# Kernel optimization log

Hardware: AMD Instinct MI355X
Metric: run time of the kernel (lower is better)

## Reference

```python
import jax, jax.numpy as jnp
import numpy as np
import math

EMBED_DIM = 1024
NUM_HEADS = 16
HEAD_DIM = EMBED_DIM // NUM_HEADS
WINDOW_SIZE = 512
BATCH = 2
SEQ_LEN = 2048


def setup_inputs() -> dict:
    key = jax.random.key(0)
    ks = jax.random.split(key, 9)
    s = 1.0 / math.sqrt(EMBED_DIM)
    inp = {
        "x": jax.random.normal(ks[0], (BATCH, SEQ_LEN, EMBED_DIM), dtype=jnp.float32),
        "Wq": jax.random.normal(ks[1], (EMBED_DIM, EMBED_DIM), dtype=jnp.float32) * s,
        "bq": jnp.zeros((EMBED_DIM,), dtype=jnp.float32),
        "Wk": jax.random.normal(ks[2], (EMBED_DIM, EMBED_DIM), dtype=jnp.float32) * s,
        "bk": jnp.zeros((EMBED_DIM,), dtype=jnp.float32),
        "Wv": jax.random.normal(ks[3], (EMBED_DIM, EMBED_DIM), dtype=jnp.float32) * s,
        "bv": jnp.zeros((EMBED_DIM,), dtype=jnp.float32),
        "Wo": jax.random.normal(ks[4], (EMBED_DIM, EMBED_DIM), dtype=jnp.float32) * s,
        "bo": jnp.zeros((EMBED_DIM,), dtype=jnp.float32),
    }
    return inp


def _sliding_window_mask(seq_len: int, window_size: int) -> jnp.ndarray:
    # mask[i, j] = 0 if |i - j| <= window_size // 2 else -inf
    i = jnp.arange(seq_len)[:, None]
    j = jnp.arange(seq_len)[None, :]
    allowed = jnp.abs(i - j) <= (window_size // 2)
    return jnp.where(allowed, 0.0, -jnp.inf).astype(jnp.float32)


def _split_heads(t):
    b, s, d = t.shape
    return t.reshape(b, s, NUM_HEADS, HEAD_DIM).transpose(0, 2, 1, 3)  # [b,h,s,hd]


def reference(x, Wq, bq, Wk, bk, Wv, bv, Wo, bo):
    b, s, d = x.shape
    q = _split_heads(x @ Wq + bq)
    k = _split_heads(x @ Wk + bk)
    v = _split_heads(x @ Wv + bv)
    # dense QK^T + additive sliding-window mask + softmax + PV (as in source)
    scores = jnp.einsum("bhqd,bhkd->bhqk", q, k) / math.sqrt(HEAD_DIM)
    scores = scores + _sliding_window_mask(s, WINDOW_SIZE)
    probs = jax.nn.softmax(scores, axis=-1)
    attn = jnp.einsum("bhqk,bhkd->bhqd", probs, v)
    attn = attn.transpose(0, 2, 1, 3).reshape(b, s, d)  # merge heads
    return attn @ Wo + bo
```

## Files before the change

### kernel.cpp

```cpp
#include <hip/hip_runtime.h>
#include <math.h>
#include <stdint.h>

#define BATCH 2
#define SEQ   2048
#define EMB   1024
#define NHEADS 16
#define HDIM  64
#define WHALF 256

typedef __attribute__((ext_vector_type(8))) short short8;
typedef __attribute__((ext_vector_type(8))) _Float16 half8;
typedef __attribute__((ext_vector_type(4))) _Float16 half4;
typedef __attribute__((ext_vector_type(4))) float f32x4;

__global__ __launch_bounds__(256)
void cast16_kernel(const float* __restrict__ in, unsigned short* __restrict__ o16, int n)
{
    const int i = (blockIdx.x * 256 + threadIdx.x) * 8;
    if (i >= n) return;
    float4 v0 = *(const float4*)&in[i];
    float4 v1 = *(const float4*)&in[i + 4];
    half8 h;
    h[0] = (_Float16)v0.x; h[1] = (_Float16)v0.y;
    h[2] = (_Float16)v0.z; h[3] = (_Float16)v0.w;
    h[4] = (_Float16)v1.x; h[5] = (_Float16)v1.y;
    h[6] = (_Float16)v1.z; h[7] = (_Float16)v1.w;
    *(half8*)&o16[i] = h;
}

__global__ __launch_bounds__(256)
void wsplit16_t_kernel(const float* __restrict__ W0, const float* __restrict__ W1,
                       const float* __restrict__ W2, const float* __restrict__ W3,
                       unsigned short* __restrict__ o16)
{
    __shared__ float t[32][33];
    const float* W = (blockIdx.z == 0) ? W0 : (blockIdx.z == 1) ? W1
                   : (blockIdx.z == 2) ? W2 : W3;
    const float scale = (blockIdx.z == 0) ? 0.125f : 1.0f;
    const int n0 = blockIdx.x * 32;
    const int k0 = blockIdx.y * 32;
    const int tx = threadIdx.x & 31, ty = threadIdx.x >> 5;
#pragma unroll
    for (int i = 0; i < 4; ++i)
        t[ty + i * 8][tx] = W[(size_t)(k0 + ty + i * 8) * EMB + n0 + tx];
    __syncthreads();
#pragma unroll
    for (int i = 0; i < 4; ++i) {
        float v = t[tx][ty + i * 8] * scale;
        size_t o = (size_t)(blockIdx.z * EMB + n0 + ty + i * 8) * EMB + k0 + tx;
        *(_Float16*)&o16[o] = (_Float16)v;
    }
}

__global__ __launch_bounds__(256)
void bias_cat_kernel(const float* __restrict__ bq, const float* __restrict__ bk,
                     const float* __restrict__ bv, float* __restrict__ out)
{
    const int i = blockIdx.x * 256 + threadIdx.x;
    if (i < 1024)      out[i] = bq[i] * 0.125f;
    else if (i < 2048) out[i] = bk[i - 1024];
    else if (i < 3072) out[i] = bv[i - 2048];
}

#define GLDS(gp, lp) __builtin_amdgcn_global_load_lds(                       \
    (const __attribute__((address_space(1))) void*)(gp),                     \
    (__attribute__((address_space(3))) void*)(lp), 16, 0, 0)

#define TRS 136

__global__ __launch_bounds__(256)
void gemm_f16_qkv_kernel(const unsigned short* __restrict__ A,
                         const unsigned short* __restrict__ B,
                         const float* __restrict__ bias,
                         _Float16* __restrict__ QK,
                         _Float16* __restrict__ Vt, int K)
{
    __shared__ __align__(16) unsigned short smem[128 * TRS];
    unsigned short* sA = smem;
    unsigned short* sB = smem + 4096;
    _Float16* tr = (_Float16*)smem;

    const int tid = threadIdx.x;
    const int l = tid & 63;
    const int w = tid >> 6;
    const int wm = w >> 1, wn = w & 1;
    const int row0 = blockIdx.y * 128;
    const int col0 = blockIdx.x * 128;

    f32x4 acc[4][4] = {};

    const int sr = tid >> 2;
    const int sk = (tid & 3) * 8;
    const unsigned short* pA = A + (size_t)(row0 + sr) * K + sk;
    const unsigned short* pB = B + (size_t)(col0 + sr) * K + sk;
    const size_t rstep = (size_t)64 * K;

    const int kq = (l >> 4) * 8;
    const int lr = l & 15;
    const int lq = l >> 4;

    for (int k0 = 0; k0 < K; k0 += 32) {
        GLDS(pA + k0,         &sA[tid * 8]);
        GLDS(pA + rstep + k0, &sA[2048 + tid * 8]);
        GLDS(pB + k0,         &sB[tid * 8]);
        GLDS(pB + rstep + k0, &sB[2048 + tid * 8]);
        __syncthreads();

        half8 af[4], bf[4];
#pragma unroll
        for (int f = 0; f < 4; ++f) {
            af[f] = *(const half8*)&sA[(wm * 64 + f * 16 + lr) * 32 + kq];
            bf[f] = *(const half8*)&sB[(wn * 64 + f * 16 + lr) * 32 + kq];
        }
#pragma unroll
        for (int mf = 0; mf < 4; ++mf)
#pragma unroll
            for (int nf = 0; nf < 4; ++nf)
                acc[mf][nf] = __builtin_amdgcn_mfma_f32_16x16x32_f16(af[mf], bf[nf], acc[mf][nf], 0, 0, 0);
        __syncthreads();
    }

    if (col0 < 2048) {
#pragma unroll
        for (int nf = 0; nf < 4; ++nf) {
            const int c = wn * 64 + nf * 16 + lr;
            const float bv = bias[col0 + c];
#pragma unroll
            for (int mf = 0; mf < 4; ++mf) {
                const int rl = wm * 64 + mf * 16 + lq * 4;
#pragma unroll
                for (int i = 0; i < 4; ++i)
                    tr[(rl + i) * TRS + c] = (_Float16)(acc[mf][nf][i] + bv);
            }
        }
        __syncthreads();
        const int r = tid >> 1, seg = (tid & 1) * 64;
        _Float16* dst = QK + (size_t)(row0 + r) * 2048 + col0 + seg;
#pragma unroll
        for (int t = 0; t < 8; ++t)
            *(half8*)&dst[t * 8] = *(const half8*)&tr[r * TRS + seg + t * 8];
    } else {
#pragma unroll
        for (int nf = 0; nf < 4; ++nf) {
            const int c = wn * 64 + nf * 16 + lr;
            const float bv = bias[col0 + c];
#pragma unroll
            for (int mf = 0; mf < 4; ++mf) {
                const int rl = wm * 64 + mf * 16 + lq * 4;
#pragma unroll
                for (int i = 0; i < 4; ++i)
                    tr[c * TRS + rl + i] = (_Float16)(acc[mf][nf][i] + bv);
            }
        }
        __syncthreads();
        const int c = tid >> 1, seg = (tid & 1) * 64;
        const int vb = row0 >> 11;
        const int s0 = (row0 & 2047) + seg;
        _Float16* dst = Vt + ((size_t)(vb * 1024 + (col0 - 2048) + c)) * 2048 + s0;
#pragma unroll
        for (int t = 0; t < 8; ++t)
            *(half8*)&dst[t * 8] = *(const half8*)&tr[c * TRS + seg + t * 8];
    }
}

__global__ __launch_bounds__(256)
void gemm_f16_m64_kernel(const unsigned short* __restrict__ A,
                         const unsigned short* __restrict__ B,
                         const float* __restrict__ bias,
                         float* __restrict__ C, int ldc, int K)
{
    __shared__ unsigned short sA[64 * 32], sB[128 * 32];

    const int tid = threadIdx.x;
    const int l = tid & 63;
    const int w = tid >> 6;
    const int wm = w >> 1, wn = w & 1;
    const int row0 = blockIdx.y * 64;
    const int col0 = blockIdx.x * 128;

    f32x4 acc[2][4] = {};

    const int sr = tid >> 2;
    const int sk = (tid & 3) * 8;
    const unsigned short* pA = A + (size_t)(row0 + sr) * K + sk;
    const unsigned short* pB = B + (size_t)(col0 + sr) * K + sk;
    const size_t rstep = (size_t)64 * K;

    const int kq = (l >> 4) * 8;
    const int lr = l & 15;
    const int lq = l >> 4;

    for (int k0 = 0; k0 < K; k0 += 32) {
        GLDS(pA + k0,         &sA[tid * 8]);
        GLDS(pB + k0,         &sB[tid * 8]);
        GLDS(pB + rstep + k0, &sB[2048 + tid * 8]);
        __syncthreads();

        half8 af[2], bf[4];
#pragma unroll
        for (int f = 0; f < 2; ++f)
            af[f] = *(const half8*)&sA[(wm * 32 + f * 16 + lr) * 32 + kq];
#pragma unroll
        for (int f = 0; f < 4; ++f)
            bf[f] = *(const half8*)&sB[(wn * 64 + f * 16 + lr) * 32 + kq];
#pragma unroll
        for (int mf = 0; mf < 2; ++mf)
#pragma unroll
            for (int nf = 0; nf < 4; ++nf)
                acc[mf][nf] = __builtin_amdgcn_mfma_f32_16x16x32_f16(af[mf], bf[nf], acc[mf][nf], 0, 0, 0);
        __syncthreads();
    }

#pragma unroll
    for (int nf = 0; nf < 4; ++nf) {
        const int c = wn * 64 + nf * 16 + lr;
        const float bv = bias[col0 + c];
#pragma unroll
        for (int mf = 0; mf < 2; ++mf) {
            const int r = row0 + wm * 32 + mf * 16 + lq * 4;
#pragma unroll
            for (int i = 0; i < 4; ++i)
                C[(size_t)(r + i) * ldc + col0 + c] = acc[mf][nf][i] + bv;
        }
    }
}

#define AP 66

__global__ __launch_bounds__(512)
void attn_f16_kernel(const unsigned short* __restrict__ QKb,
                     const unsigned short* __restrict__ Vt,
                     unsigned short* __restrict__ Oa)
{
    __shared__ unsigned short Qs[128 * AP], Ks[64 * AP], Vs[64 * AP], Ps[128 * AP];

    const int tid = threadIdx.x;
    const int gid = blockIdx.x;
    const int X = gid & 7, rest = gid >> 3;
    const int hg = rest & 3, tile = rest >> 2;
    const int bh = X * 4 + hg;
    const int b = bh >> 4, h = bh & 15;
    const int q0 = tile * 128;

    const int l = tid & 63, w = tid >> 6;
    const int lr = l & 15, g = l >> 4;

    const size_t rowbase = (size_t)b * SEQ;

    {
        const int r = tid >> 2, sg = (tid & 3) * 16;
        const unsigned short* src = QKb + (rowbase + q0 + r) * 2048 + h * HDIM + sg;
        *(short8*)&Qs[r * AP + sg]     = *(const short8*)src;
        *(short8*)&Qs[r * AP + sg + 8] = *(const short8*)(src + 8);
    }
    __syncthreads();

    half8 qa0 = *(const half8*)&Qs[(w * 16 + lr) * AP + g * 8];
    half8 qa1 = *(const half8*)&Qs[(w * 16 + lr) * AP + 32 + g * 8];

    f32x4 o[4] = {};
    float m_ = -1e30f, l_ = 0.0f;
    const int q = q0 + w * 16 + lr;

    const int c_begin = (q0 >= WHALF) ? 0 : (WHALF - q0) >> 6;
    int c_end = (SEQ + 255 - q0) >> 6; if (c_end > 9) c_end = 9;

    for (int c = c_begin; c <= c_end; ++c) {
        const int cs = q0 - WHALF + c * 64;

        {
            const int r = tid >> 3, sg = (tid & 7) * 8;
            const unsigned short* ks = QKb + (rowbase + cs + r) * 2048 + 1024 + h * HDIM + sg;
            *(short8*)&Ks[r * AP + sg] = *(const short8*)ks;
            const unsigned short* vs = Vt + ((size_t)(b * 1024 + h * HDIM + r)) * 2048 + cs + sg;
            *(short8*)&Vs[r * AP + sg] = *(const short8*)vs;
        }
        __syncthreads();

        f32x4 sc[4] = {};
#pragma unroll
        for (int kf = 0; kf < 4; ++kf) {
            half8 a0 = *(const half8*)&Ks[(kf * 16 + lr) * AP + g * 8];
            half8 a1 = *(const half8*)&Ks[(kf * 16 + lr) * AP + 32 + g * 8];
            sc[kf] = __builtin_amdgcn_mfma_f32_16x16x32_f16(a0, qa0, sc[kf], 0, 0, 0);
            sc[kf] = __builtin_amdgcn_mfma_f32_16x16x32_f16(a1, qa1, sc[kf], 0, 0, 0);
        }

        if (c <= 1) {
#pragma unroll
            for (int kf = 0; kf < 4; ++kf)
#pragma unroll
                for (int i = 0; i < 4; ++i) {
                    const int key = cs + kf * 16 + g * 4 + i;
                    if (key < q - WHALF) sc[kf][i] = -1e30f;
                }
        } else if (c >= 8) {
#pragma unroll
            for (int kf = 0; kf < 4; ++kf)
#pragma unroll
                for (int i = 0; i < 4; ++i) {
                    const int key = cs + kf * 16 + g * 4 + i;
                    if (key > q + WHALF) sc[kf][i] = -1e30f;
                }
        }

        float cm = sc[0][0];
#pragma unroll
        for (int kf = 0; kf < 4; ++kf)
#pragma unroll
            for (int i = 0; i < 4; ++i) cm = fmaxf(cm, sc[kf][i]);
        cm = fmaxf(cm, __shfl_xor(cm, 16));
        cm = fmaxf(cm, __shfl_xor(cm, 32));

        const float mn = fmaxf(fmaxf(m_, cm), -1e4f);
        const float alpha = __expf(m_ - mn);
        m_ = mn;

        float rs = 0.0f;
#pragma unroll
        for (int kf = 0; kf < 4; ++kf) {
            half4 pk;
#pragma unroll
            for (int i = 0; i < 4; ++i) {
                const float p = __expf(sc[kf][i] - mn);
                rs += p;
                pk[i] = (_Float16)p;
            }
            *(half4*)&Ps[(w * 16 + lr) * AP + kf * 16 + g * 4] = pk;
        }
        rs += __shfl_xor(rs, 16);
        rs += __shfl_xor(rs, 32);
        l_ = l_ * alpha + rs;

        float al[4];
#pragma unroll
        for (int i = 0; i < 4; ++i)
            al[i] = __shfl(alpha, (l & 48) | (g * 4 + i));
#pragma unroll
        for (int df = 0; df < 4; ++df)
#pragma unroll
            for (int i = 0; i < 4; ++i) o[df][i] *= al[i];

        half8 pa0 = *(const half8*)&Ps[(w * 16 + lr) * AP + g * 8];
        half8 pa1 = *(const half8*)&Ps[(w * 16 + lr) * AP + 32 + g * 8];
#pragma unroll
        for (int df = 0; df < 4; ++df) {
            half8 vb0 = *(const half8*)&Vs[(df * 16 + lr) * AP + g * 8];
            half8 vb1 = *(const half8*)&Vs[(df * 16 + lr) * AP + 32 + g * 8];
            o[df] = __builtin_amdgcn_mfma_f32_16x16x32_f16(pa0, vb0, o[df], 0, 0, 0);
            o[df] = __builtin_amdgcn_mfma_f32_16x16x32_f16(pa1, vb1, o[df], 0, 0, 0);
        }
        __syncthreads();
    }

    float invl[4];
#pragma unroll
    for (int i = 0; i < 4; ++i)
        invl[i] = 1.0f / __shfl(l_, (l & 48) | (g * 4 + i));
#pragma unroll
    for (int df = 0; df < 4; ++df)
#pragma unroll
        for (int i = 0; i < 4; ++i) {
            const float v = o[df][i] * invl[i];
            const size_t off = (rowbase + q0 + w * 16 + g * 4 + i) * 1024
                             + h * HDIM + df * 16 + lr;
            *(_Float16*)&Oa[off] = (_Float16)v;
        }
}

#define BM 64
#define BN 64
#define BK 16

__global__ __launch_bounds__(256)
void gemm_bias_kernel(const float* __restrict__ A, const float* __restrict__ W,
                      const float* __restrict__ bias, float* __restrict__ C,
                      int M, int N, int K)
{
    __shared__ float As[BK][BM + 4];
    __shared__ float Bs[BK][BN + 4];
    const int tid = threadIdx.x;
    const int tx = tid & 15, ty = tid >> 4;
    const int row0 = blockIdx.y * BM;
    const int col0 = blockIdx.x * BN;
    float acc[4][4] = {};
    const int ar = tid >> 2;
    const int ak = (tid & 3) * 4;
    const int br = tid >> 4;
    const int bc = (tid & 15) * 4;
    for (int k0 = 0; k0 < K; k0 += BK) {
        float4 a = *(const float4*)&A[(size_t)(row0 + ar) * K + k0 + ak];
        float4 b = *(const float4*)&W[(size_t)(k0 + br) * N + col0 + bc];
        As[ak + 0][ar] = a.x; As[ak + 1][ar] = a.y;
        As[ak + 2][ar] = a.z; As[ak + 3][ar] = a.w;
        *(float4*)&Bs[br][bc] = b;
        __syncthreads();
#pragma unroll
        for (int kk = 0; kk < BK; ++kk) {
            float4 av = *(const float4*)&As[kk][ty * 4];
            float4 bv = *(const float4*)&Bs[kk][tx * 4];
            float aa[4] = {av.x, av.y, av.z, av.w};
            float bb[4] = {bv.x, bv.y, bv.z, bv.w};
#pragma unroll
            for (int i = 0; i < 4; ++i)
#pragma unroll
                for (int j = 0; j < 4; ++j)
                    acc[i][j] = fmaf(aa[i], bb[j], acc[i][j]);
        }
        __syncthreads();
    }
    const float4 bvec = *(const float4*)&bias[col0 + tx * 4];
    const float bb[4] = {bvec.x, bvec.y, bvec.z, bvec.w};
#pragma unroll
    for (int i = 0; i < 4; ++i) {
        float4 oo;
        oo.x = acc[i][0] + bb[0]; oo.y = acc[i][1] + bb[1];
        oo.z = acc[i][2] + bb[2]; oo.w = acc[i][3] + bb[3];
        *(float4*)&C[(size_t)(row0 + ty * 4 + i) * N + col0 + tx * 4] = oo;
    }
}

#define QT 32
#define KT 64

__global__ __launch_bounds__(256)
void attn_kernel(const float* __restrict__ Qm, int ldq,
                 const float* __restrict__ Km, int ldk,
                 const float* __restrict__ Vm, int ldv,
                 float* __restrict__ Om, int ldo)
{
    __shared__ float Qs[QT][HDIM + 4];
    __shared__ float KVs[KT][HDIM + 4];
    __shared__ float Ps[QT][KT + 1];
    __shared__ float red[8][QT];
    __shared__ float m_s[QT], l_s[QT], alpha_s[QT];
    const int tid = threadIdx.x;
    const int b  = blockIdx.y / NHEADS;
    const int h  = blockIdx.y % NHEADS;
    const int q0 = blockIdx.x * QT;
    const int r  = tid & 31;
    const int cg = tid >> 5;
    const int d0 = cg * 8;
    {
        const int qr = tid >> 3;
        const int qd = (tid & 7) * 8;
        const float* src = Qm + (size_t)(b * SEQ + q0 + qr) * ldq + h * HDIM + qd;
        *(float4*)&Qs[qr][qd]     = *(const float4*)(src);
        *(float4*)&Qs[qr][qd + 4] = *(const float4*)(src + 4);
    }
    if (tid < QT) { m_s[tid] = -1e30f; l_s[tid] = 0.0f; }
    __syncthreads();
    float qreg[HDIM];
#pragma unroll
    for (int d4 = 0; d4 < HDIM; d4 += 4) {
        float4 t = *(const float4*)&Qs[r][d4];
        qreg[d4] = t.x; qreg[d4 + 1] = t.y; qreg[d4 + 2] = t.z; qreg[d4 + 3] = t.w;
    }
    float o[8] = {};
    const int iq = q0 + r;
    int lo = q0 - WHALF; if (lo < 0) lo = 0;
    const int cs0 = lo & ~(KT - 1);
    int hi = q0 + QT + WHALF; if (hi > SEQ) hi = SEQ;
    const int nch = (hi - cs0 + KT - 1) / KT;
    const int kr0 = tid >> 4;
    const int kc  = (tid & 15) * 4;
    for (int ch = 0; ch < nch; ++ch) {
        const int cs = cs0 + ch * KT;
#pragma unroll
        for (int r4 = 0; r4 < 4; ++r4) {
            const int row = kr0 + r4 * 16;
            const int j = cs + row;
            float4 v = make_float4(0.f, 0.f, 0.f, 0.f);
            if (j < SEQ)
                v = *(const float4*)&Km[(size_t)(b * SEQ + j) * ldk + h * HDIM + kc];
            *(float4*)&KVs[row][kc] = v;
        }
        __syncthreads();
        float s[8];
#pragma unroll
        for (int cc = 0; cc < 8; ++cc) {
            const int cidx = d0 + cc;
            float acc = 0.0f;
#pragma unroll
            for (int d4 = 0; d4 < HDIM; d4 += 4) {
                float4 kv = *(const float4*)&KVs[cidx][d4];
                acc = fmaf(qreg[d4],     kv.x, acc);
                acc = fmaf(qreg[d4 + 1], kv.y, acc);
                acc = fmaf(qreg[d4 + 2], kv.z, acc);
                acc = fmaf(qreg[d4 + 3], kv.w, acc);
            }
            const int j = cs + cidx;
            const bool valid = (j < SEQ) && (j >= iq - WHALF) && (j <= iq + WHALF);
            s[cc] = valid ? acc * 0.125f : -1e30f;
        }
        float lm = s[0];
#pragma unroll
        for (int cc = 1; cc < 8; ++cc) lm = fmaxf(lm, s[cc]);
        red[cg][r] = lm;
        __syncthreads();
        if (tid < QT) {
            float m = m_s[tid];
            float mc = red[0][tid];
#pragma unroll
            for (int g2 = 1; g2 < 8; ++g2) mc = fmaxf(mc, red[g2][tid]);
            const float mn = fmaxf(m, mc);
            alpha_s[tid] = __expf(m - mn);
            m_s[tid] = mn;
        }
        __syncthreads();
        const float mn = m_s[r];
        float ls = 0.0f;
#pragma unroll
        for (int cc = 0; cc < 8; ++cc) {
            const float p = __expf(s[cc] - mn);
            Ps[r][d0 + cc] = p;
            ls += p;
        }
        red[cg][r] = ls;
        __syncthreads();
        if (tid < QT) {
            float sum = red[0][tid];
#pragma unroll
            for (int g2 = 1; g2 < 8; ++g2) sum += red[g2][tid];
            l_s[tid] = l_s[tid] * alpha_s[tid] + sum;
        }
#pragma unroll
        for (int r4 = 0; r4 < 4; ++r4) {
            const int row = kr0 + r4 * 16;
            const int j = cs + row;
            float4 v = make_float4(0.f, 0.f, 0.f, 0.f);
            if (j < SEQ)
                v = *(const float4*)&Vm[(size_t)(b * SEQ + j) * ldv + h * HDIM + kc];
            *(float4*)&KVs[row][kc] = v;
        }
        {
            const float al = alpha_s[r];
#pragma unroll
            for (int dd = 0; dd < 8; ++dd) o[dd] *= al;
        }
        __syncthreads();
        for (int j = 0; j < KT; ++j) {
            const float p = Ps[r][j];
            float4 v0 = *(const float4*)&KVs[j][d0];
            float4 v1 = *(const float4*)&KVs[j][d0 + 4];
            o[0] = fmaf(p, v0.x, o[0]); o[1] = fmaf(p, v0.y, o[1]);
            o[2] = fmaf(p, v0.z, o[2]); o[3] = fmaf(p, v0.w, o[3]);
            o[4] = fmaf(p, v1.x, o[4]); o[5] = fmaf(p, v1.y, o[5]);
            o[6] = fmaf(p, v1.z, o[6]); o[7] = fmaf(p, v1.w, o[7]);
        }
        __syncthreads();
    }
    const float inv = 1.0f / l_s[r];
    float4 o0, o1;
    o0.x = o[0] * inv; o0.y = o[1] * inv; o0.z = o[2] * inv; o0.w = o[3] * inv;
    o1.x = o[4] * inv; o1.y = o[5] * inv; o1.z = o[6] * inv; o1.w = o[7] * inv;
    float* dst = Om + (size_t)(b * SEQ + q0 + r) * ldo + h * HDIM + d0;
    *(float4*)dst       = o0;
    *(float4*)(dst + 4) = o1;
}

extern "C" void kernel_launch(void* const* d_in, const int* in_sizes, int n_in,
                              void* d_out, int out_size, void* d_ws, size_t ws_size,
                              hipStream_t stream)
{
    const float* x  = (const float*)d_in[0];
    const float* Wq = (const float*)d_in[1];
    const float* bq = (const float*)d_in[2];
    const float* Wk = (const float*)d_in[3];
    const float* bk = (const float*)d_in[4];
    const float* Wv = (const float*)d_in[5];
    const float* bv = (const float*)d_in[6];
    const float* Wo = (const float*)d_in[7];
    const float* bo = (const float*)d_in[8];
    float* out = (float*)d_out;

    const int M = BATCH * SEQ;
    const size_t MK = (size_t)M * EMB;

    const size_t need = ((size_t)40 << 20) + 16384;
    dim3 blk(256);

    if (ws_size >= need) {
        unsigned short* Wh  = (unsigned short*)d_ws;
        unsigned short* xh  = Wh + (size_t)4096 * EMB;
        unsigned short* QKb = xh + MK;
        unsigned short* Vt  = QKb + (size_t)4096 * 2048;
        unsigned short* Oa  = xh;
        float* bias_cat = (float*)((char*)d_ws + ((size_t)40 << 20));

        hipLaunchKernelGGL(cast16_kernel, dim3((int)(MK / (256 * 8))), blk, 0, stream,
                           x, xh, (int)MK);
        hipLaunchKernelGGL(wsplit16_t_kernel, dim3(32, 32, 4), blk, 0, stream,
                           Wq, Wk, Wv, Wo, Wh);
        hipLaunchKernelGGL(bias_cat_kernel, dim3(12), blk, 0, stream, bq, bk, bv, bias_cat);

        hipLaunchKernelGGL(gemm_f16_qkv_kernel, dim3(24, 32), blk, 0, stream,
                           xh, Wh, bias_cat, (_Float16*)QKb, (_Float16*)Vt, EMB);

        hipLaunchKernelGGL(attn_f16_kernel, dim3(512), dim3(512), 0, stream, QKb, Vt, Oa);

        hipLaunchKernelGGL(gemm_f16_m64_kernel, dim3(8, 64), blk, 0, stream,
                           Oa, Wh + (size_t)3072 * EMB, bo, out, EMB, EMB);
    } else {
        float* Qb = (float*)d_ws;
        float* Kb = Qb + MK;
        float* Vb = out;
        dim3 ggrid(EMB / BN, M / BM);
        hipLaunchKernelGGL(gemm_bias_kernel, ggrid, blk, 0, stream, x, Wq, bq, Qb, M, EMB, EMB);
        hipLaunchKernelGGL(gemm_bias_kernel, ggrid, blk, 0, stream, x, Wk, bk, Kb, M, EMB, EMB);
        hipLaunchKernelGGL(gemm_bias_kernel, ggrid, blk, 0, stream, x, Wv, bv, Vb, M, EMB, EMB);
        hipLaunchKernelGGL(attn_kernel, dim3(SEQ / QT, BATCH * NHEADS), blk, 0, stream,
                           Qb, EMB, Kb, EMB, Vb, EMB, Qb, EMB);
        hipLaunchKernelGGL(gemm_bias_kernel, ggrid, blk, 0, stream, Qb, Wo, bo, out, M, EMB, EMB);
    }
}
```

Before: 207.9 us.

## Widen GEMM K-step to 64 and register-prefetch K/V tiles in attention

Both GEMM kernels now stage two 32-wide K slices per iteration, halving the number of barrier pairs per K sweep at the cost of doubled LDS tiles. The attention kernel loads the next K/V chunk into registers while the current chunk is computed, hiding global latency behind the MFMA work. It also aliases the P buffer onto the Q staging buffer to cut LDS use and raise occupancy. The aliasing is only safe if Q is no longer read from shared memory after the Q fragments are loaded into registers.

```diff
diff --git a/kernel.cpp b/kernel.cpp
--- a/kernel.cpp
+++ b/kernel.cpp
@@ -78,7 +78,7 @@
 {
     __shared__ __align__(16) unsigned short smem[128 * TRS];
     unsigned short* sA = smem;
-    unsigned short* sB = smem + 4096;
+    unsigned short* sB = smem + 8192;
     _Float16* tr = (_Float16*)smem;
 
     const int tid = threadIdx.x;
@@ -100,24 +100,33 @@
     const int lr = l & 15;
     const int lq = l >> 4;
 
-    for (int k0 = 0; k0 < K; k0 += 32) {
-        GLDS(pA + k0,         &sA[tid * 8]);
-        GLDS(pA + rstep + k0, &sA[2048 + tid * 8]);
-        GLDS(pB + k0,         &sB[tid * 8]);
-        GLDS(pB + rstep + k0, &sB[2048 + tid * 8]);
-        __syncthreads();
-
-        half8 af[4], bf[4];
-#pragma unroll
-        for (int f = 0; f < 4; ++f) {
-            af[f] = *(const half8*)&sA[(wm * 64 + f * 16 + lr) * 32 + kq];
-            bf[f] = *(const half8*)&sB[(wn * 64 + f * 16 + lr) * 32 + kq];
-        }
-#pragma unroll
-        for (int mf = 0; mf < 4; ++mf)
-#pragma unroll
-            for (int nf = 0; nf < 4; ++nf)
-                acc[mf][nf] = __builtin_amdgcn_mfma_f32_16x16x32_f16(af[mf], bf[nf], acc[mf][nf], 0, 0, 0);
+    for (int k0 = 0; k0 < K; k0 += 64) {
+        GLDS(pA + k0,              &sA[tid * 8]);
+        GLDS(pA + rstep + k0,      &sA[2048 + tid * 8]);
+        GLDS(pA + k0 + 32,         &sA[4096 + tid * 8]);
+        GLDS(pA + rstep + k0 + 32, &sA[6144 + tid * 8]);
+        GLDS(pB + k0,              &sB[tid * 8]);
+        GLDS(pB + rstep + k0,      &sB[2048 + tid * 8]);
+        GLDS(pB + k0 + 32,         &sB[4096 + tid * 8]);
+        GLDS(pB + rstep + k0 + 32, &sB[6144 + tid * 8]);
+        __syncthreads();
+
+#pragma unroll
+        for (int s = 0; s < 2; ++s) {
+            const unsigned short* a0 = sA + s * 4096;
+            const unsigned short* b0 = sB + s * 4096;
+            half8 af[4], bf[4];
+#pragma unroll
+            for (int f = 0; f < 4; ++f) {
+                af[f] = *(const half8*)&a0[(wm * 64 + f * 16 + lr) * 32 + kq];
+                bf[f] = *(const half8*)&b0[(wn * 64 + f * 16 + lr) * 32 + kq];
+            }
+#pragma unroll
+            for (int mf = 0; mf < 4; ++mf)
+#pragma unroll
+                for (int nf = 0; nf < 4; ++nf)
+                    acc[mf][nf] = __builtin_amdgcn_mfma_f32_16x16x32_f16(af[mf], bf[nf], acc[mf][nf], 0, 0, 0);
+        }
         __syncthreads();
     }
 
@@ -170,7 +179,7 @@
                          const float* __restrict__ bias,
                          float* __restrict__ C, int ldc, int K)
 {
-    __shared__ unsigned short sA[64 * 32], sB[128 * 32];
+    __shared__ unsigned short sA[2 * 64 * 32], sB[2 * 128 * 32];
 
     const int tid = threadIdx.x;
     const int l = tid & 63;
@@ -191,24 +200,32 @@
     const int lr = l & 15;
     const int lq = l >> 4;
 
-    for (int k0 = 0; k0 < K; k0 += 32) {
-        GLDS(pA + k0,         &sA[tid * 8]);
-        GLDS(pB + k0,         &sB[tid * 8]);
-        GLDS(pB + rstep + k0, &sB[2048 + tid * 8]);
-        __syncthreads();
-
-        half8 af[2], bf[4];
-#pragma unroll
-        for (int f = 0; f < 2; ++f)
-            af[f] = *(const half8*)&sA[(wm * 32 + f * 16 + lr) * 32 + kq];
-#pragma unroll
-        for (int f = 0; f < 4; ++f)
-            bf[f] = *(const half8*)&sB[(wn * 64 + f * 16 + lr) * 32 + kq];
-#pragma unroll
-        for (int mf = 0; mf < 2; ++mf)
-#pragma unroll
-            for (int nf = 0; nf < 4; ++nf)
-                acc[mf][nf] = __builtin_amdgcn_mfma_f32_16x16x32_f16(af[mf], bf[nf], acc[mf][nf], 0, 0, 0);
+    for (int k0 = 0; k0 < K; k0 += 64) {
+        GLDS(pA + k0,              &sA[tid * 8]);
+        GLDS(pA + k0 + 32,         &sA[2048 + tid * 8]);
+        GLDS(pB + k0,              &sB[tid * 8]);
+        GLDS(pB + rstep + k0,      &sB[2048 + tid * 8]);
+        GLDS(pB + k0 + 32,         &sB[4096 + tid * 8]);
+        GLDS(pB + rstep + k0 + 32, &sB[6144 + tid * 8]);
+        __syncthreads();
+
+#pragma unroll
+        for (int s = 0; s < 2; ++s) {
+            const unsigned short* a0 = sA + s * 2048;
+            const unsigned short* b0 = sB + s * 4096;
+            half8 af[2], bf[4];
+#pragma unroll
+            for (int f = 0; f < 2; ++f)
+                af[f] = *(const half8*)&a0[(wm * 32 + f * 16 + lr) * 32 + kq];
+#pragma unroll
+            for (int f = 0; f < 4; ++f)
+                bf[f] = *(const half8*)&b0[(wn * 64 + f * 16 + lr) * 32 + kq];
+#pragma unroll
+            for (int mf = 0; mf < 2; ++mf)
+#pragma unroll
+                for (int nf = 0; nf < 4; ++nf)
+                    acc[mf][nf] = __builtin_amdgcn_mfma_f32_16x16x32_f16(af[mf], bf[nf], acc[mf][nf], 0, 0, 0);
+        }
         __syncthreads();
     }
 
@@ -233,7 +250,8 @@
                      const unsigned short* __restrict__ Vt,
                      unsigned short* __restrict__ Oa)
 {
-    __shared__ unsigned short Qs[128 * AP], Ks[64 * AP], Vs[64 * AP], Ps[128 * AP];
+    __shared__ unsigned short Qs[128 * AP], Ks[64 * AP], Vs[64 * AP];
+    unsigned short* Ps = Qs;
 
     const int tid = threadIdx.x;
     const int gid = blockIdx.x;
@@ -266,17 +284,26 @@
     const int c_begin = (q0 >= WHALF) ? 0 : (WHALF - q0) >> 6;
     int c_end = (SEQ + 255 - q0) >> 6; if (c_end > 9) c_end = 9;
 
+    const int sr_ = tid >> 3, sg_ = (tid & 7) * 8;
+    short8 kreg, vreg;
+    {
+        const int cs = q0 - WHALF + c_begin * 64;
+        kreg = *(const short8*)(QKb + (rowbase + cs + sr_) * 2048 + 1024 + h * HDIM + sg_);
+        vreg = *(const short8*)(Vt + ((size_t)(b * 1024 + h * HDIM + sr_)) * 2048 + cs + sg_);
+    }
+
     for (int c = c_begin; c <= c_end; ++c) {
         const int cs = q0 - WHALF + c * 64;
 
-        {
-            const int r = tid >> 3, sg = (tid & 7) * 8;
-            const unsigned short* ks = QKb + (rowbase + cs + r) * 2048 + 1024 + h * HDIM + sg;
-            *(short8*)&Ks[r * AP + sg] = *(const short8*)ks;
-            const unsigned short* vs = Vt + ((size_t)(b * 1024 + h * HDIM + r)) * 2048 + cs + sg;
-            *(short8*)&Vs[r * AP + sg] = *(const short8*)vs;
-        }
-        __syncthreads();
+        *(short8*)&Ks[sr_ * AP + sg_] = kreg;
+        *(short8*)&Vs[sr_ * AP + sg_] = vreg;
+        __syncthreads();
+
+        if (c < c_end) {
+            const int cs2 = cs + 64;
+            kreg = *(const short8*)(QKb + (rowbase + cs2 + sr_) * 2048 + 1024 + h * HDIM + sg_);
+            vreg = *(const short8*)(Vt + ((size_t)(b * 1024 + h * HDIM + sr_)) * 2048 + cs2 + sg_);
+        }
 
         f32x4 sc[4] = {};
 #pragma unroll
```

Result: slower. 213.9 us (+2.9%).
